# Kernel tuning notes

Hardware: AMD Instinct MI355X
Metric: run time of the kernel (lower is better)

Reference implementation:

```python
import jax, jax.numpy as jnp
import numpy as np

DIM = 128; DSTATE = 64; DHEAD = 64; EXPAND = 2
DINNER = EXPAND * DIM; NH = DINNER // DHEAD
CONVK = 4; CHUNK = 128
BATCH = 1; DD = 32; HH = 32; WW = 32
CONVCH = DINNER + 2 * DSTATE
DPROJ = 2 * DINNER + 2 * DSTATE + NH


def rmsnorm(v, w, eps=1e-6):
    return v * jax.lax.rsqrt(jnp.mean(v * v, axis=-1, keepdims=True) + eps) * w


def ssd(xh, dt, A, Bm, Cm):
    # chunked SSD selective scan. xh [b,l,h,p], dt [b,l,h], A [h], Bm/Cm [b,l,n]
    b, l, h, p = xh.shape
    n = Bm.shape[-1]
    c, k = l // CHUNK, CHUNK
    dA = (dt * A).reshape(b, c, k, h)
    xdt = (xh * dt[..., None]).reshape(b, c, k, h, p)
    Bm = Bm.reshape(b, c, k, n)
    Cm = Cm.reshape(b, c, k, n)
    cum = jnp.cumsum(dA, axis=2)                  # [b,c,k,h] inclusive
    cum_h = cum.transpose(0, 1, 3, 2)             # [b,c,h,k]
    tri = jnp.tril(jnp.ones((k, k), bool))
    Lmat = jnp.exp(jnp.where(tri, cum_h[..., :, None] - cum_h[..., None, :], -jnp.inf))
    CB = jnp.einsum('bctn,bcsn->bcts', Cm, Bm)
    Y_intra = jnp.einsum('bcts,bchts,bcshp->bcthp', CB, Lmat, xdt)
    decay_end = jnp.exp(cum[:, :, -1:, :] - cum)  # [b,c,k,h]
    S = jnp.einsum('bcsn,bcsh,bcshp->bchpn', Bm, decay_end, xdt)
    cdec = jnp.exp(cum[:, :, -1])                 # [b,c,h]

    def step(hprev, inp):
        s_c, dec = inp
        return dec[:, :, None, None] * hprev + s_c, hprev

    init = jnp.zeros((b, h, p, n), xh.dtype)
    _, hprevs = jax.lax.scan(step, init, (S.transpose(1, 0, 2, 3, 4), cdec.transpose(1, 0, 2)))
    hprevs = hprevs.transpose(1, 0, 2, 3, 4)      # [b,c,h,p,n] state at each chunk start
    Y_inter = jnp.einsum('bctn,bcth,bchpn->bcthp', Cm, jnp.exp(cum), hprevs)
    return (Y_intra + Y_inter).reshape(b, l, h, p)


def mamba2(x, Win, convw, convb, dtb, Alog, Dp, normw, Wout):
    b, l, _ = x.shape
    zxbcdt = x @ Win
    z = zxbcdt[..., :DINNER]
    xBC = zxbcdt[..., DINNER:DINNER + CONVCH]
    dt = zxbcdt[..., DINNER + CONVCH:]
    xc = xBC.transpose(0, 2, 1)
    xc = jax.lax.conv_general_dilated(xc, convw, (1,), [(CONVK - 1, 0)],
                                      dimension_numbers=('NCH', 'OIH', 'NCH'),
                                      feature_group_count=CONVCH)
    xBC = jax.nn.silu(xc + convb[None, :, None]).transpose(0, 2, 1)
    xh = xBC[..., :DINNER].reshape(b, l, NH, DHEAD)
    Bm = xBC[..., DINNER:DINNER + DSTATE]
    Cm = xBC[..., DINNER + DSTATE:]
    dt = jax.nn.softplus(dt + dtb)
    A = -jnp.exp(Alog)
    y = ssd(xh, dt, A, Bm, Cm) + Dp[None, None, :, None] * xh
    y = y.reshape(b, l, DINNER)
    y = rmsnorm(y * jax.nn.silu(z), normw)
    return y @ Wout


def ss3d(xn, gate_w, gate_b, ps, pn, pz):
    B, D, H, W, C = xn.shape
    x_s = xn.reshape(B, -1, C)
    x_n = jnp.transpose(xn, (0, 2, 1, 3, 4)).reshape(B, -1, C)
    x_z = jnp.transpose(xn, (0, 3, 1, 2, 4)).reshape(B, -1, C)
    o_sf = mamba2(x_s, *ps).reshape(B, D, H, W, C)
    o_sb = jnp.flip(mamba2(jnp.flip(x_s, 1), *ps), 1).reshape(B, D, H, W, C)
    o_nf = mamba2(x_n, *pn).reshape(B, H, D, W, C).transpose(0, 2, 1, 3, 4)
    o_nb = jnp.flip(mamba2(jnp.flip(x_n, 1), *pn), 1).reshape(B, H, D, W, C).transpose(0, 2, 1, 3, 4)
    o_zf = mamba2(x_z, *pz).reshape(B, W, D, H, C).transpose(0, 2, 3, 1, 4)
    o_zb = jnp.flip(mamba2(jnp.flip(x_z, 1), *pz), 1).reshape(B, W, D, H, C).transpose(0, 2, 3, 1, 4)
    stack = jnp.stack([o_sf, o_sb, o_nf, o_nb, o_zf, o_zb], axis=1)  # [B,6,D,H,W,C]
    gates = jax.nn.softmax(xn @ gate_w + gate_b, axis=-1)            # [B,D,H,W,6]
    gates = jnp.transpose(gates[..., None], (0, 4, 1, 2, 3, 5))      # [B,6,D,H,W,1]
    return (stack * gates).sum(axis=1)


def block(x, norm_w, gate_w, gate_b, ps, pn, pz, loc_dw_w, loc_dw_b, loc_pw_w, loc_pw_b,
          ca_w1, ca_b1, ca_w2, ca_b2, alpha):
    xp = jnp.transpose(x, (0, 2, 3, 4, 1))
    xn = rmsnorm(xp, norm_w)
    g = jnp.transpose(ss3d(xn, gate_w, gate_b, ps, pn, pz), (0, 4, 1, 2, 3))
    xcf = jnp.transpose(xn, (0, 4, 1, 2, 3))
    lc = jax.lax.conv_general_dilated(xcf, loc_dw_w, (1, 1, 1), [(1, 1)] * 3,
                                      dimension_numbers=('NCDHW', 'OIDHW', 'NCDHW'),
                                      feature_group_count=DIM) + loc_dw_b[None, :, None, None, None]
    lc = jax.nn.silu(jnp.einsum('bcdhw,oc->bodhw', lc, loc_pw_w) + loc_pw_b[None, :, None, None, None])
    fused = alpha * g + (1.0 - alpha) * lc
    yc = jnp.mean(fused, axis=(2, 3, 4), keepdims=True)
    yc = jnp.einsum('bcdhw,oc->bodhw', yc, ca_w1) + ca_b1[None, :, None, None, None]
    yc = jnp.where(yc >= 0, yc, 0.1 * yc)  # LeakyReLU(0.1)
    yc = jnp.einsum('bcdhw,oc->bodhw', yc, ca_w2) + ca_b2[None, :, None, None, None]
    return x + fused * jax.nn.sigmoid(yc)


def setup_inputs() -> dict:
    keys = iter(jax.random.split(jax.random.key(0), 64))

    def rn(shape, s=1.0):
        return jax.random.normal(next(keys), shape, jnp.float32) * s

    inp = {"x": rn((BATCH, DIM, DD, HH, WW))}
    inp["norm_w"] = jnp.ones((DIM,)) + rn((DIM,), 0.02)
    inp["gate_w"] = rn((DIM, 6), 0.02)
    inp["gate_b"] = jnp.zeros((6,))
    for m in ("s", "n", "zm"):
        inp[m + "_Win"] = rn((DIM, DPROJ), 0.02)
        inp[m + "_convw"] = rn((CONVCH, 1, CONVK), 0.2)
        inp[m + "_convb"] = jnp.zeros((CONVCH,))
        inp[m + "_dtb"] = rn((NH,), 0.3)
        inp[m + "_Alog"] = jnp.log(jnp.arange(1, NH + 1, dtype=jnp.float32))
        inp[m + "_D"] = jnp.ones((NH,))
        inp[m + "_normw"] = jnp.ones((DINNER,))
        inp[m + "_Wout"] = rn((DINNER, DIM), 0.02)
    inp["loc_dw_w"] = rn((DIM, 1, 3, 3, 3), 0.1)
    inp["loc_dw_b"] = jnp.zeros((DIM,))
    inp["loc_pw_w"] = rn((DIM, DIM), 0.05)
    inp["loc_pw_b"] = jnp.zeros((DIM,))
    inp["ca_w1"] = rn((DIM // 16, DIM), 0.05)
    inp["ca_b1"] = jnp.zeros((DIM // 16,))
    inp["ca_w2"] = rn((DIM, DIM // 16), 0.05)
    inp["ca_b2"] = jnp.zeros((DIM,))
    inp["alpha"] = jnp.array(0.5, jnp.float32)
    return inp


def reference(x, norm_w, gate_w, gate_b,
              s_Win, s_convw, s_convb, s_dtb, s_Alog, s_D, s_normw, s_Wout,
              n_Win, n_convw, n_convb, n_dtb, n_Alog, n_D, n_normw, n_Wout,
              zm_Win, zm_convw, zm_convb, zm_dtb, zm_Alog, zm_D, zm_normw, zm_Wout,
              loc_dw_w, loc_dw_b, loc_pw_w, loc_pw_b, ca_w1, ca_b1, ca_w2, ca_b2, alpha):
    ps = (s_Win, s_convw, s_convb, s_dtb, s_Alog, s_D, s_normw, s_Wout)
    pn = (n_Win, n_convw, n_convb, n_dtb, n_Alog, n_D, n_normw, n_Wout)
    pz = (zm_Win, zm_convw, zm_convb, zm_dtb, zm_Alog, zm_D, zm_normw, zm_Wout)
    return block(x, norm_w, gate_w, gate_b, ps, pn, pz,
                 loc_dw_w, loc_dw_b, loc_pw_w, loc_pw_b, ca_w1, ca_b1, ca_w2, ca_b2, alpha)
```

## Files before the change

### kernel.cpp

```cpp
#include <hip/hip_runtime.h>


typedef unsigned short u16;
typedef unsigned int   u32;
typedef __attribute__((ext_vector_type(8))) short short8;
typedef __attribute__((ext_vector_type(8))) _Float16 half8;
typedef __attribute__((ext_vector_type(4))) float f32x4;

#define LSEQ 32768
#define CDIM 128
#define NPROJ 644
#define ZXS 672
#define CCH 384
#define DIN 256
#define NHD 4
#define CKL 128
#define NCHK 256

__device__ __forceinline__ float b2f(u16 u){ u32 x=((u32)u)<<16; float f; __builtin_memcpy(&f,&x,4); return f; }
__device__ __forceinline__ u16 f2b(float f){ u32 x; __builtin_memcpy(&x,&f,4); x += 0x7fffu + ((x>>16)&1u); return (u16)(x>>16); }
__device__ __forceinline__ u16 f2h(float v){ _Float16 h=(_Float16)v; u16 b; __builtin_memcpy(&b,&h,2); return b; }
__device__ __forceinline__ float h2f(u16 b){ _Float16 h; __builtin_memcpy(&h,&b,2); return (float)h; }
__device__ __forceinline__ void up4(uint2 v, float* o){
  union { uint2 u; _Float16 h[4]; } c; c.u = v;
  o[0]=(float)c.h[0]; o[1]=(float)c.h[1]; o[2]=(float)c.h[2]; o[3]=(float)c.h[3];
}
__device__ __forceinline__ uint2 pk4(const float* o){
  union { uint2 u; _Float16 h[4]; } c;
  c.h[0]=(_Float16)o[0]; c.h[1]=(_Float16)o[1]; c.h[2]=(_Float16)o[2]; c.h[3]=(_Float16)o[3];
  return c.u;
}
__device__ __forceinline__ float sigmoidf_(float v){ return 1.f/(1.f+__expf(-v)); }
__device__ __forceinline__ float siluf_(float v){ return v*sigmoidf_(v); }
__device__ __forceinline__ float softplusf_(float v){ return (v>20.f)? v : log1pf(__expf(v)); }

__device__ __forceinline__ int seq2sp(int t, int run){
  int te = (run&1) ? (LSEQ-1-t) : t;
  int a = te>>10, b=(te>>5)&31, c=te&31;
  int d,h,w;
  switch(run>>1){
    case 0: d=a; h=b; w=c; break;
    case 1: h=a; d=b; w=c; break;
    default: w=a; d=b; h=c; break;
  }
  return (d<<10)|(h<<5)|w;
}

__global__ void k_xn(const float* __restrict__ x, const float* __restrict__ nw,
                     const float* __restrict__ gw, const float* __restrict__ gb,
                     float* __restrict__ XN, float* __restrict__ G){
  int s = blockIdx.x*256 + threadIdx.x;
  float ss = 0.f;
  #pragma unroll 8
  for (int c=0;c<CDIM;c++){ float v=x[c*LSEQ+s]; ss += v*v; }
  float sc = rsqrtf(ss*(1.f/CDIM)+1e-6f);
  float a[6];
  #pragma unroll
  for (int j=0;j<6;j++) a[j]=gb[j];
  #pragma unroll 8
  for (int c=0;c<CDIM;c++){
    float v = x[c*LSEQ+s]*sc*nw[c];
    XN[c*LSEQ+s] = v;
    #pragma unroll
    for (int j=0;j<6;j++) a[j] += v*gw[c*6+j];
  }
  float m=a[0];
  #pragma unroll
  for (int j=1;j<6;j++) m = fmaxf(m,a[j]);
  float e[6], ssum=0.f;
  #pragma unroll
  for (int j=0;j<6;j++){ e[j]=__expf(a[j]-m); ssum+=e[j]; }
  float inv = 1.f/ssum;
  #pragma unroll
  for (int j=0;j<6;j++) G[j*LSEQ+s] = e[j]*inv;
}

__global__ __launch_bounds__(256) void k_permprep(const float* __restrict__ XN, u16* __restrict__ XNT, int dir,
                                                  const float* __restrict__ Win, const float* __restrict__ Wout,
                                                  u16* __restrict__ WinT, u16* __restrict__ WoT){
  __shared__ u16 TS[128*34];
  int bid = blockIdx.x;
  int tid = threadIdx.x;
  if (bid < 1024){
    int a = bid>>5, b = bid&31;
    int spa = (dir==1)? b : a;
    int spb = (dir==1)? a : b;
    int spbase = spa*1024 + spb*32;
    for (int idx=tid; idx<4096; idx+=256){
      int c = idx>>5, i = idx&31;
      TS[c*34+i] = f2b(XN[c*LSEQ + spbase + i]);
    }
    __syncthreads();
    for (int idx=tid; idx<4096; idx+=256){
      int i = idx>>7, c = idx&127;
      int t = (dir==2) ? (i*1024 + a*32 + b) : (a*1024 + b*32 + i);
      XNT[t*128 + c] = TS[c*34+i];
    }
  } else if (bid < 1408){
    int idx = (bid-1024)*256 + tid;
    int j = idx>>7, k = idx&127;
    float v = (j<NPROJ)? Win[k*NPROJ + j] : 0.f;
    WinT[idx] = f2b(v);
  } else {
    int idx = (bid-1408)*256 + tid;
    int c = idx>>8, k = idx&255;
    WoT[idx] = f2h(Wout[k*CDIM + c]);
  }
}

__global__ __launch_bounds__(256) void k_gin_mfma(const u16* __restrict__ XNT, const u16* __restrict__ WinT,
                                                  u16* __restrict__ ZX, int flip){
  __shared__ u16 Asb[128*136];
  __shared__ u16 Bsb[128*136];
  int g = blockIdx.x;
  int w = (g&7)*192 + (g>>3);
  int by = w/6, bx = w - by*6;
  int j0 = bx*128, t0 = by*128;
  int tid = threadIdx.x;
  for (int ch = tid; ch < 2048; ch += 256){
    int row = ch>>4, c8 = ch&15;
    int tg = flip ? (LSEQ-1-(t0+row)) : (t0+row);
    uint4 av = *(const uint4*)(XNT + tg*128 + c8*8);
    *(uint4*)(&Asb[row*136 + c8*8]) = av;
    uint4 bv = *(const uint4*)(WinT + (j0+row)*128 + c8*8);
    *(uint4*)(&Bsb[row*136 + c8*8]) = bv;
  }
  __syncthreads();
  int lane = tid&63, wid = tid>>6;
  int wm = (wid>>1)*64, wn = (wid&1)*64;
  int lm = lane&15, lq = lane>>4;
  f32x4 acc[4][4] = {};
  for (int kt=0; kt<4; kt++){
    short8 af[4], bf[4];
    #pragma unroll
    for (int mt=0;mt<4;mt++) af[mt] = *(const short8*)(&Asb[(wm+mt*16+lm)*136 + kt*32 + lq*8]);
    #pragma unroll
    for (int nt=0;nt<4;nt++) bf[nt] = *(const short8*)(&Bsb[(wn+nt*16+lm)*136 + kt*32 + lq*8]);
    #pragma unroll
    for (int mt=0;mt<4;mt++)
      #pragma unroll
      for (int nt=0;nt<4;nt++)
        acc[mt][nt] = __builtin_amdgcn_mfma_f32_16x16x32_bf16(af[mt], bf[nt], acc[mt][nt], 0,0,0);
  }
  __syncthreads();
  #pragma unroll
  for (int mt=0;mt<4;mt++)
    #pragma unroll
    for (int nt=0;nt<4;nt++)
      #pragma unroll
      for (int r=0;r<4;r++)
        Asb[(wm+mt*16+lq*4+r)*136 + wn+nt*16+lm] = f2h(acc[mt][nt][r]);
  __syncthreads();
  if (bx < 5){
    for (int idx=tid; idx<2048; idx+=256){
      int row = idx>>4, q = idx&15;
      *(uint4*)(ZX + (t0+row)*ZXS + j0 + q*8) = *(const uint4*)(&Asb[row*136 + q*8]);
    }
  } else {
    for (int idx=tid; idx<128; idx+=256){
      *(uint2*)(ZX + (t0+idx)*ZXS + j0) = *(const uint2*)(&Asb[idx*136]);
    }
  }
}

__global__ __launch_bounds__(384) void k_convdt(const u16* __restrict__ ZX, const float* __restrict__ cw,
                                                const float* __restrict__ cb, u16* __restrict__ XB,
                                                const float* __restrict__ dtb, const float* __restrict__ Alog,
                                                float* __restrict__ DT, float* __restrict__ CUM,
                                                float* __restrict__ CDEC, float* __restrict__ DE){
  __shared__ u16 smc[35*384];
  int bid = blockIdx.x;
  int tid = threadIdx.x;
  if (bid < 1024){
    int t0 = bid*32;
    for (int idx=tid; idx<13440; idx+=384){
      int j = idx/384, chh = idx - j*384;
      int t = t0-3+j;
      smc[idx] = (t>=0)? ZX[t*ZXS + 256 + chh] : (u16)0;
    }
    __syncthreads();
    int ch = tid;
    float w0=cw[ch*4], w1=cw[ch*4+1], w2=cw[ch*4+2], w3=cw[ch*4+3], bb=cb[ch];
    for (int i=0;i<32;i++){
      float acc = w0*h2f(smc[i*384+ch]) + w1*h2f(smc[(i+1)*384+ch])
                + w2*h2f(smc[(i+2)*384+ch]) + w3*h2f(smc[(i+3)*384+ch]) + bb;
      XB[(t0+i)*CCH + ch] = f2h(siluf_(acc));
    }
  } else if (tid < 256){
    int g = (bid-1024)*4 + (tid>>6);
    int lane = tid&63;
    int c = g>>2, h = g&3;
    float A = -__expf(Alog[h]);
    float bias = dtb[h];
    int t0 = c*CKL + lane*2;
    float x0 = h2f(ZX[t0*ZXS + 640 + h]);
    float x1 = h2f(ZX[(t0+1)*ZXS + 640 + h]);
    float d0 = softplusf_(x0+bias), d1 = softplusf_(x1+bias);
    DT[t0*4+h] = d0; DT[(t0+1)*4+h] = d1;
    float e0 = d0*A, e1 = d1*A;
    float s = e0+e1;
    #pragma unroll
    for (int off=1; off<64; off<<=1){
      float v = __shfl_up(s, off, 64);
      if (lane>=off) s += v;
    }
    float c0 = s - e1, c1 = s;
    CUM[t0*4+h] = c0;
    CUM[(t0+1)*4+h] = c1;
    float tot = __shfl(s, 63, 64);
    DE[t0*4+h]     = __expf(tot - c0);
    DE[(t0+1)*4+h] = __expf(tot - c1);
    if (lane==0) CDEC[c*4+h] = __expf(tot);
  }
}

__global__ __launch_bounds__(256,4) void k_chunk(const u16* __restrict__ XB, const float* __restrict__ DT,
                                                 const float* __restrict__ CUM, const float* __restrict__ DE,
                                                 const float* __restrict__ Dp,
                                                 u16* __restrict__ YA, u16* __restrict__ ST){
  __shared__ u16 sh[19968];
  u16* R0   = sh;
  u16* Mtri = sh;
  u16* Xsh  = sh + 11264;
  u16* scr  = sh;

  int bid = blockIdx.x; int c = bid&255, h = bid>>8;
  int tid = threadIdx.x, lane = tid&63, wid = tid>>6;
  int lm = lane&15, lq = lane>>4;
  const u16* XBc = XB + c*CKL*CCH;
  const float* DTc = DT + c*CKL*4 + h;
  const float* DEc = DE + c*CKL*4 + h;

  for (int idx=tid; idx<4096; idx+=256){
    int t2 = idx>>6, n = idx&63, t = t2*2;
    const u16* r0 = XBc + t*CCH;
    float dt0 = DTc[t*4], dt1 = DTc[(t+1)*4];
    u32 xp = (u32)f2h(h2f(r0[(h<<6)+n])*dt0) | ((u32)f2h(h2f(r0[CCH+(h<<6)+n])*dt1)<<16);
    *(u32*)&Xsh[n*136 + t] = xp;
    float de0 = DEc[t*4], de1 = DEc[(t+1)*4];
    u32 bp = (u32)f2h(h2f(r0[256+n])*de0) | ((u32)f2h(h2f(r0[CCH+256+n])*de1)<<16);
    *(u32*)&R0[n*136 + t] = bp;
  }
  if (tid<128) ((float*)(Xsh + (tid>>1)*136 + 128))[tid&1] = CUM[(c*CKL+tid)*4 + h];
  __syncthreads();
  #define CUMS(t) (((const float*)(Xsh + ((t)>>1)*136 + 128))[(t)&1])

  f32x4 sa[4] = {};
  #pragma unroll
  for (int kt=0; kt<4; kt++){
    half8 aa = *(const half8*)&Xsh[(wid*16+lm)*136 + kt*32 + lq*8];
    #pragma unroll
    for (int nt=0;nt<4;nt++){
      half8 bq = *(const half8*)&R0[(nt*16+lm)*136 + kt*32 + lq*8];
      sa[nt] = __builtin_amdgcn_mfma_f32_16x16x32_f16(aa, bq, sa[nt], 0,0,0);
    }
  }
  #pragma unroll
  for (int nt=0;nt<4;nt++){
    int n = nt*16 + lm;
    #pragma unroll
    for (int r=0;r<4;r++){
      int p = wid*16 + lq*4 + r;
      ST[((c*4+h)*64 + p)*64 + n] = f2h(sa[nt][r]);
    }
  }

  int sp0 = wid, sp1 = 7 - wid;
  f32x4 cbA[4] = {};
  f32x4 cbB[8] = {};
  const u16* lanebase = XBc + lm*CCH + lq*8;
  #pragma unroll
  for (int kt=0; kt<2; kt++){
    half8 afA = *(const half8*)(lanebase + sp0*16*CCH + 320 + kt*32);
    half8 afB = *(const half8*)(lanebase + sp1*16*CCH + 320 + kt*32);
    #pragma unroll
    for (int st=0; st<8; st++){
      if (st <= sp1){
        half8 bq = *(const half8*)(lanebase + st*16*CCH + 256 + kt*32);
        if (st <= sp0)
          cbA[st&3] = __builtin_amdgcn_mfma_f32_16x16x32_f16(afA, bq, cbA[st&3], 0,0,0);
        cbB[st] = __builtin_amdgcn_mfma_f32_16x16x32_f16(afB, bq, cbB[st], 0,0,0);
      }
    }
  }
  __syncthreads();

  float dval = Dp[h];
  u16 outv[2][4][4];
  #pragma unroll
  for (int i=0;i<2;i++){
    int sp_ = i ? sp1 : sp0;
    int q = sp_ >> 1;
    int Wst = 32*q + 40;
    int mb  = 16*(32*q*q + 48*q + (sp_&1)*(32*q+40));
    u16* Mrow = Mtri + mb;
    float ct[4];
    #pragma unroll
    for (int r=0;r<4;r++) ct[r] = CUMS(sp_*16 + lq*4 + r);

    #pragma unroll
    for (int st=0; st<8; st++){
      if (st <= sp_){
        int s = st*16 + lm;
        float cs = CUMS(s);
        f32x4 cb;
        if (i==0) cb = cbA[st&3]; else cb = cbB[st];
        if (st == sp_){
          #pragma unroll
          for (int r=0;r<4;r++){
            int t = sp_*16 + lq*4 + r;
            float m = (s <= t) ? cb[r]*__expf(ct[r]-cs) : 0.f;
            Mrow[(lq*4+r)*Wst + s] = f2h(m);
          }
          if (!(sp_&1)){
            #pragma unroll
            for (int r=0;r<4;r++) Mrow[(lq*4+r)*Wst + s + 16] = 0;
          }
        } else {
          #pragma unroll
          for (int r=0;r<4;r++)
            Mrow[(lq*4+r)*Wst + s] = f2h(cb[r]*__expf(ct[r]-cs));
        }
      }
    }

    f32x4 ya[4] = {};
    int nkt = q + 1;
    #pragma unroll
    for (int kt=0; kt<4; kt++){
      if (kt < nkt){
        half8 af = *(const half8*)&Mrow[lm*Wst + kt*32 + lq*8];
        #pragma unroll
        for (int nt=0;nt<4;nt++){
          half8 bq = *(const half8*)&Xsh[(nt*16+lm)*136 + kt*32 + lq*8];
          ya[nt] = __builtin_amdgcn_mfma_f32_16x16x32_f16(af, bq, ya[nt], 0,0,0);
        }
      }
    }

    #pragma unroll
    for (int nt=0;nt<4;nt++){
      int p = nt*16 + lm;
      #pragma unroll
      for (int r=0;r<4;r++){
        int t = sp_*16 + lq*4 + r;
        float xhv = h2f(XBc[t*CCH + (h<<6) + p]);
        outv[i][nt][r] = f2h(ya[nt][r] + dval*xhv);
      }
    }
  }
  __syncthreads();

  #pragma unroll
  for (int i=0;i<2;i++){
    int sp_ = i ? sp1 : sp0;
    #pragma unroll
    for (int nt=0;nt<4;nt++)
      #pragma unroll
      for (int r=0;r<4;r++)
        scr[(sp_*16+lq*4+r)*68 + nt*16+lm] = outv[i][nt][r];
  }
  __syncthreads();
  for (int idx=tid; idx<2048; idx+=256){
    int row = idx>>4, q = idx&15;
    *(uint2*)(YA + ((c*CKL+row)<<8) + (h<<6) + q*4) = *(const uint2*)(&scr[row*68 + q*4]);
  }
  #undef CUMS
}

__global__ __launch_bounds__(256) void k_scan(const u16* __restrict__ ST, u16* __restrict__ HP,
                                              const float* __restrict__ CDEC){
  __shared__ float L[4][64][64];
  __shared__ float E[4][64];
  int tid = threadIdx.x;
  int j = tid>>6, s = tid&63;
  int b = blockIdx.x;
  int g = b*64 + s;
  int h = g>>12;
  int a = j*64;
  float hloc = 0.f;
  #pragma unroll 16
  for (int i=0;i<64;i++){
    int c = a+i;
    L[j][i][s] = hloc;
    hloc = CDEC[(c<<2)+h]*hloc + h2f(ST[g + (c<<14)]);
  }
  E[j][s] = hloc;
  __syncthreads();
  float carry = 0.f;
  for (int k=0;k<j;k++){
    float P = 1.f;
    #pragma unroll 16
    for (int i=0;i<64;i++) P *= CDEC[((k*64+i)<<2)+h];
    carry = E[k][s] + P*carry;
  }
  float m = 1.f;
  #pragma unroll 16
  for (int i=0;i<64;i++){
    int c = a+i;
    HP[g + (c<<14)] = f2h(L[j][i][s] + m*carry);
    m *= CDEC[(c<<2)+h];
  }
}

__global__ __launch_bounds__(256) void k_inter(const u16* __restrict__ XB, const float* __restrict__ CUM,
                                               const u16* __restrict__ HP, u16* __restrict__ YB){
  __shared__ u16 Cs[128*72];
  __shared__ u16 Hs[4*64*72];
  __shared__ float ex_s[4*128];
  int c = blockIdx.x;
  int tid = threadIdx.x, lane = tid&63, wid = tid>>6;
  int lm = lane&15, lq = lane>>4;
  for (int idx=tid; idx<1024; idx+=256){
    int t = idx>>3, b8 = idx&7;
    *(uint4*)&Cs[t*72 + b8*8] = *(const uint4*)(XB + (c*CKL+t)*CCH + 320 + b8*8);
  }
  for (int idx=tid; idx<2048; idx+=256){
    int h = idx>>9, p = (idx>>3)&63, b8 = idx&7;
    *(uint4*)&Hs[(h*64+p)*72 + b8*8] = *(const uint4*)(HP + ((c*4+h)*64+p)*64 + b8*8);
  }
  for (int idx=tid; idx<512; idx+=256){
    int h = idx>>7, t = idx&127;
    ex_s[h*128+t] = __expf(CUM[(c*CKL+t)*4+h]);
  }
  __syncthreads();
  int h = wid;
  const u16* Hh = &Hs[h*64*72];
  f32x4 acc[8][4] = {};
  for (int kt=0; kt<2; kt++){
    half8 af[8], bfv[4];
    #pragma unroll
    for (int mt=0;mt<8;mt++) af[mt] = *(const half8*)&Cs[(mt*16+lm)*72 + kt*32 + lq*8];
    #pragma unroll
    for (int nt=0;nt<4;nt++) bfv[nt] = *(const half8*)&Hh[(nt*16+lm)*72 + kt*32 + lq*8];
    #pragma unroll
    for (int mt=0;mt<8;mt++)
      #pragma unroll
      for (int nt=0;nt<4;nt++)
        acc[mt][nt] = __builtin_amdgcn_mfma_f32_16x16x32_f16(af[mt], bfv[nt], acc[mt][nt], 0,0,0);
  }
  #pragma unroll
  for (int mt=0;mt<8;mt++){
    #pragma unroll
    for (int r=0;r<4;r++){
      int t = mt*16 + lq*4 + r;
      float e = ex_s[h*128+t];
      u16* dst = &YB[((c*CKL+t)<<8) + (h<<6)];
      #pragma unroll
      for (int nt=0;nt<4;nt++){
        int p = nt*16 + lm;
        dst[p] = f2h(e*acc[mt][nt][r]);
      }
    }
  }
}

__global__ __launch_bounds__(256) void k_gout_mfma(const u16* __restrict__ YA, const u16* __restrict__ YB,
                                                   const u16* __restrict__ ZX, const float* __restrict__ nw,
                                                   const u16* __restrict__ WoT,
                                                   const float* __restrict__ G, float* __restrict__ GACC, int run){
  __shared__ u16 Ys[128*136];
  __shared__ u16 Ws[128*136];
  __shared__ float SSs[128];
  int t0 = blockIdx.x*128;
  int tid = threadIdx.x, lane = tid&63, wid = tid>>6;
  int lm = lane&15, lq = lane>>4;
  f32x4 acc[2][8] = {};
  for (int kb=0; kb<2; kb++){
    __syncthreads();
    for (int ch=tid; ch<2048; ch+=256){
      int row = ch>>4, c8 = ch&15;
      int t = t0+row;
      int cb = kb*128 + c8*8;
      uint2 av0 = *(const uint2*)(YA + t*DIN + cb);
      uint2 av1 = *(const uint2*)(YA + t*DIN + cb + 4);
      uint2 bv0 = *(const uint2*)(YB + t*DIN + cb);
      uint2 bv1 = *(const uint2*)(YB + t*DIN + cb + 4);
      uint2 zv0 = *(const uint2*)(ZX + t*ZXS + cb);
      uint2 zv1 = *(const uint2*)(ZX + t*ZXS + cb + 4);
      float af[8], bf[8], zf[8];
      up4(av0, af); up4(av1, af+4);
      up4(bv0, bf); up4(bv1, bf+4);
      up4(zv0, zf); up4(zv1, zf+4);
      float ssp = 0.f;
      union { uint4 u; u16 h[8]; } pk;
      #pragma unroll
      for (int j=0;j<8;j++){
        float u = (af[j]+bf[j])*siluf_(zf[j]);
        ssp += u*u;
        pk.h[j] = f2h(u*nw[cb+j]);
      }
      *(uint4*)&Ys[row*136 + c8*8] = pk.u;
      *(uint4*)&Ws[row*136 + c8*8] = *(const uint4*)(WoT + row*DIN + kb*128 + c8*8);
      #pragma unroll
      for (int off=1; off<16; off<<=1) ssp += __shfl_xor(ssp, off, 64);
      if ((lane&15)==0){ if (kb==0) SSs[row] = ssp; else SSs[row] += ssp; }
    }
    __syncthreads();
    for (int kt=0; kt<4; kt++){
      half8 af[2], bfv[8];
      #pragma unroll
      for (int mt=0;mt<2;mt++) af[mt] = *(const half8*)&Ys[(wid*32+mt*16+lm)*136 + kt*32 + lq*8];
      #pragma unroll
      for (int nt=0;nt<8;nt++) bfv[nt] = *(const half8*)&Ws[(nt*16+lm)*136 + kt*32 + lq*8];
      #pragma unroll
      for (int mt=0;mt<2;mt++)
        #pragma unroll
        for (int nt=0;nt<8;nt++)
          acc[mt][nt] = __builtin_amdgcn_mfma_f32_16x16x32_f16(af[mt], bfv[nt], acc[mt][nt], 0,0,0);
    }
  }
  #pragma unroll
  for (int mt=0;mt<2;mt++){
    #pragma unroll
    for (int r=0;r<4;r++){
      int tl = wid*32 + mt*16 + lq*4 + r;
      int t = t0 + tl;
      int sp = seq2sp(t, run);
      float sc = rsqrtf(SSs[tl]*(1.f/DIN)+1e-6f);
      float g = G[run*LSEQ + sp] * sc;
      float* dst = &GACC[sp*CDIM];
      if (run==0){
        #pragma unroll
        for (int nt=0;nt<8;nt++) dst[nt*16+lm] = g*acc[mt][nt][r];
      } else {
        #pragma unroll
        for (int nt=0;nt<8;nt++) dst[nt*16+lm] += g*acc[mt][nt][r];
      }
    }
  }
}

__global__ __launch_bounds__(256) void k_dwconv(const float* __restrict__ XN, const float* __restrict__ w,
                                                const float* __restrict__ b, float* __restrict__ LC1){
  __shared__ float sm[3*34*40];
  int cc = blockIdx.x>>5, d = blockIdx.x&31;
  int tid = threadIdx.x;
  for (int i=tid; i<4080; i+=256) sm[i] = 0.f;
  __syncthreads();
  #pragma unroll
  for (int p=0;p<3;p++){
    int dz = d-1+p;
    if ((unsigned)dz<=31u){
      for (int idx=tid; idx<1024; idx+=256){
        int hh = idx>>5, ww = idx&31;
        sm[p*1360 + (hh+1)*40 + (ww+4)] = XN[cc*LSEQ + (dz<<10) + idx];
      }
    }
  }
  __syncthreads();
  float wreg[27];
  #pragma unroll
  for (int i=0;i<27;i++) wreg[i] = w[cc*27+i];
  float bias = b[cc];
  int h = tid>>3, w0 = (tid&7)*4;
  float4 acc = {bias,bias,bias,bias};
  #pragma unroll
  for (int p=0;p<3;p++){
    #pragma unroll
    for (int dy=0;dy<3;dy++){
      const float* row = &sm[p*1360 + (h+dy)*40 + 4];
      float left  = row[w0-1];
      float4 mid  = *(const float4*)&row[w0];
      float right = row[w0+4];
      float wa=wreg[p*9+dy*3+0], wb=wreg[p*9+dy*3+1], wc=wreg[p*9+dy*3+2];
      acc.x += wa*left  + wb*mid.x + wc*mid.y;
      acc.y += wa*mid.x + wb*mid.y + wc*mid.z;
      acc.z += wa*mid.y + wb*mid.z + wc*mid.w;
      acc.w += wa*mid.z + wb*mid.w + wc*right;
    }
  }
  *(float4*)&LC1[cc*LSEQ + (d<<10) + h*32 + w0] = acc;
}

__global__ __launch_bounds__(256) void k_pw(const float* __restrict__ LC1, const float* __restrict__ pw,
                                            const float* __restrict__ pwb, float* __restrict__ LC2){
  __shared__ u16 Ws[128*136];
  __shared__ u16 Bs[128*136];
  int s0 = blockIdx.x*128;
  int tid = threadIdx.x, lane = tid&63, wid = tid>>6;
  int lm = lane&15, lq = lane>>4;
  for (int idx=tid; idx<16384; idx+=256){
    int o = idx>>7, cc = idx&127;
    Ws[o*136+cc] = f2h(pw[idx]);
  }
  for (int idx=tid; idx<16384; idx+=256){
    int cc = idx>>7, n = idx&127;
    Bs[n*136+cc] = f2h(LC1[cc*LSEQ + s0 + n]);
  }
  __syncthreads();
  f32x4 acc[2][8] = {};
  for (int kt=0; kt<4; kt++){
    half8 af[2], bfv[8];
    #pragma unroll
    for (int mt=0;mt<2;mt++) af[mt] = *(const half8*)&Ws[(wid*32+mt*16+lm)*136 + kt*32 + lq*8];
    #pragma unroll
    for (int nt=0;nt<8;nt++) bfv[nt] = *(const half8*)&Bs[(nt*16+lm)*136 + kt*32 + lq*8];
    #pragma unroll
    for (int mt=0;mt<2;mt++)
      #pragma unroll
      for (int nt=0;nt<8;nt++)
        acc[mt][nt] = __builtin_amdgcn_mfma_f32_16x16x32_f16(af[mt], bfv[nt], acc[mt][nt], 0,0,0);
  }
  #pragma unroll
  for (int mt=0;mt<2;mt++){
    #pragma unroll
    for (int r=0;r<4;r++){
      int o = wid*32 + mt*16 + lq*4 + r;
      float bb = pwb[o];
      float* dst = &LC2[o*LSEQ + s0];
      #pragma unroll
      for (int nt=0;nt<8;nt++){
        int n = nt*16 + lm;
        dst[n] = siluf_(acc[mt][nt][r] + bb);
      }
    }
  }
}

__global__ void k_fuse(const float* __restrict__ GACC, const float* __restrict__ LC2,
                       const float* __restrict__ alpha, float* __restrict__ FUSED,
                       float* __restrict__ MEANP){
  __shared__ float tile[64*65];
  int bs = blockIdx.x>>1, bc = blockIdx.x&1;
  int s0 = bs*64, c0 = bc*64;
  int tid = threadIdx.x;
  float a = alpha[0];
  for (int idx=tid; idx<4096; idx+=256){
    int i = idx>>6, j = idx&63;
    tile[i*65+j] = GACC[(s0+i)*CDIM + c0+j];
  }
  __syncthreads();
  for (int idx=tid; idx<4096; idx+=256){
    int j = idx>>6, i = idx&63;
    float g = tile[i*65+j];
    float l = LC2[(c0+j)*LSEQ + s0+i];
    float f = a*g + (1.f-a)*l;
    FUSED[(c0+j)*LSEQ + s0+i] = f;
    float wsum = f;
    #pragma unroll
    for (int off=32; off; off>>=1) wsum += __shfl_xor(wsum, off, 64);
    if ((tid&63)==0) MEANP[(c0+j)*512 + bs] = wsum;
  }
}

__global__ void k_ca(const float* __restrict__ MEANP, const float* __restrict__ w1, const float* __restrict__ b1,
                     const float* __restrict__ w2, const float* __restrict__ b2, float* __restrict__ SIG){
  __shared__ float MEANsh[128];
  __shared__ float y1[8];
  int tid = threadIdx.x;
  {
    float acc = 0.f;
    const float* p = MEANP + tid*512;
    #pragma unroll 16
    for (int b=0;b<512;b++) acc += p[b];
    MEANsh[tid] = acc*(1.f/LSEQ);
  }
  __syncthreads();
  if (tid<8){
    float acc = b1[tid];
    for (int c=0;c<128;c++) acc += w1[tid*128+c]*MEANsh[c];
    y1[tid] = (acc>=0.f)? acc : 0.1f*acc;
  }
  __syncthreads();
  float acc = b2[tid];
  #pragma unroll
  for (int o=0;o<8;o++) acc += w2[tid*8+o]*y1[o];
  SIG[tid] = sigmoidf_(acc);
}

__global__ void k_final(const float* __restrict__ x, const float* __restrict__ F, const float* __restrict__ SIG,
                        float* __restrict__ out){
  int idx = blockIdx.x*256 + threadIdx.x;
  int cc = idx>>15;
  out[idx] = x[idx] + F[idx]*SIG[cc];
}

extern "C" void kernel_launch(void* const* d_in, const int* in_sizes, int n_in,
                              void* d_out, int out_size, void* d_ws, size_t ws_size,
                              hipStream_t stream){
  (void)in_sizes; (void)n_in; (void)out_size; (void)ws_size;
  const float* x       = (const float*)d_in[0];
  const float* norm_w  = (const float*)d_in[1];
  const float* gate_w  = (const float*)d_in[2];
  const float* gate_b  = (const float*)d_in[3];
  const float* loc_dw_w= (const float*)d_in[28];
  const float* loc_dw_b= (const float*)d_in[29];
  const float* loc_pw_w= (const float*)d_in[30];
  const float* loc_pw_b= (const float*)d_in[31];
  const float* ca_w1   = (const float*)d_in[32];
  const float* ca_b1   = (const float*)d_in[33];
  const float* ca_w2   = (const float*)d_in[34];
  const float* ca_b2   = (const float*)d_in[35];
  const float* alpha   = (const float*)d_in[36];

  float* W     = (float*)d_ws;
  float* XN    = W;
  float* GATES = XN    + 4194304;
  float* GACC  = GATES + 196608;
  u16*   ZX    = (u16*)(GACC + 4194304);
  u16*   XB    = (u16*)(GACC + 4194304 + 11010048);
  float* DT    = GACC + 4194304 + 11010048 + 6291456;
  float* CUM   = DT    + 131072;
  float* CDEC  = CUM   + 131072;
  float* DE    = CDEC  + 1024;
  float* STreg = DE    + 131072;
  float* Y     = STreg + 4194304;
  float* LC1   = Y     + 8388608;
  float* LC2   = LC1   + 4194304;
  float* MEANP = LC2   + 4194304;
  float* SIG   = MEANP + 65536;
  u16*   XNT   = (u16*)(SIG + 128);
  u16*   WinT  = XNT + 4194304;
  u16*   WoT   = WinT + 98304;
  u16*   ST16  = (u16*)STreg;
  u16*   YA    = (u16*)Y;
  u16*   YB    = YA + 8388608;
  u16*   HP16  = (u16*)LC1;

  k_xn<<<128,256,0,stream>>>(x, norm_w, gate_w, gate_b, XN, GATES);

  for (int r=0;r<6;r++){
    int m = r>>1;
    const float* Win   = (const float*)d_in[4 + m*8 + 0];
    const float* convw = (const float*)d_in[4 + m*8 + 1];
    const float* convb = (const float*)d_in[4 + m*8 + 2];
    const float* dtb   = (const float*)d_in[4 + m*8 + 3];
    const float* Alog  = (const float*)d_in[4 + m*8 + 4];
    const float* Dp    = (const float*)d_in[4 + m*8 + 5];
    const float* nw2   = (const float*)d_in[4 + m*8 + 6];
    const float* Wout  = (const float*)d_in[4 + m*8 + 7];
    if ((r&1)==0){
      k_permprep<<<1536,256,0,stream>>>(XN, XNT, m, Win, Wout, WinT, WoT);
    }
    k_gin_mfma<<<1536,256,0,stream>>>(XNT, WinT, ZX, r&1);
    k_convdt  <<<1280,384,0,stream>>>(ZX, convw, convb, XB, dtb, Alog, DT, CUM, CDEC, DE);
    k_chunk   <<<1024,256,0,stream>>>(XB, DT, CUM, DE, Dp, YA, ST16);
    k_scan    <<<256,256,0,stream>>>(ST16, HP16, CDEC);
    k_inter   <<<256,256,0,stream>>>(XB, CUM, HP16, YB);
    k_gout_mfma<<<256,256,0,stream>>>(YA, YB, ZX, nw2, WoT, GATES, GACC, r);
  }

  k_dwconv<<<4096,256,0,stream>>>(XN, loc_dw_w, loc_dw_b, LC1);
  k_pw    <<<256,256,0,stream>>>(LC1, loc_pw_w, loc_pw_b, LC2);
  k_fuse  <<<1024,256,0,stream>>>(GACC, LC2, alpha, LC1, MEANP);
  k_ca    <<<1,128,0,stream>>>(MEANP, ca_w1, ca_b1, ca_w2, ca_b2, SIG);
  k_final <<<16384,256,0,stream>>>(x, LC1, SIG, (float*)d_out);
}
```

Before: 910.5 us.

## Fuse inter-chunk output kernel with gated norm and output projection

Merges k_inter and k_gout_mfma into one kernel, so the inter-chunk Y contribution stays in shared memory instead of being written to and re-read from a global YB buffer. Shared memory is aliased between phases, and the second half of heads is staged after the first kb pass. WoT fragments are now read directly from global memory rather than staged in LDS. This saves one launch and a large fp16 round trip per run. The costs are extra syncs, higher register pressure from holding both accumulators, and uncached global B-operand loads.

```diff
diff --git a/kernel.cpp b/kernel.cpp
--- a/kernel.cpp
+++ b/kernel.cpp
@@ -403,17 +403,26 @@
   }
 }
 
-__global__ __launch_bounds__(256) void k_inter(const u16* __restrict__ XB, const float* __restrict__ CUM,
-                                               const u16* __restrict__ HP, u16* __restrict__ YB){
-  __shared__ u16 Cs[128*72];
-  __shared__ u16 Hs[4*64*72];
-  __shared__ float ex_s[4*128];
+__global__ __launch_bounds__(256,2) void k_intergout(const u16* __restrict__ XB, const float* __restrict__ CUM,
+                                                     const u16* __restrict__ HP,
+                                                     const u16* __restrict__ YA, const u16* __restrict__ ZX,
+                                                     const float* __restrict__ nw, const u16* __restrict__ WoT,
+                                                     const float* __restrict__ G, float* __restrict__ GACC, int run){
+  __shared__ u16 sh[34304];
+  __shared__ float ex_s[512];
+  __shared__ float SSs[128];
+  u16* Cs  = sh;
+  u16* Hs  = sh + 9216;
+  u16* Ybs = sh;
+  u16* Ys  = sh + 16896;
   int c = blockIdx.x;
   int tid = threadIdx.x, lane = tid&63, wid = tid>>6;
   int lm = lane&15, lq = lane>>4;
+  int t0 = c*CKL;
+
   for (int idx=tid; idx<1024; idx+=256){
     int t = idx>>3, b8 = idx&7;
-    *(uint4*)&Cs[t*72 + b8*8] = *(const uint4*)(XB + (c*CKL+t)*CCH + 320 + b8*8);
+    *(uint4*)&Cs[t*72 + b8*8] = *(const uint4*)(XB + (t0+t)*CCH + 320 + b8*8);
   }
   for (int idx=tid; idx<2048; idx+=256){
     int h = idx>>9, p = (idx>>3)&63, b8 = idx&7;
@@ -421,111 +430,119 @@
   }
   for (int idx=tid; idx<512; idx+=256){
     int h = idx>>7, t = idx&127;
-    ex_s[h*128+t] = __expf(CUM[(c*CKL+t)*4+h]);
-  }
-  __syncthreads();
-  int h = wid;
-  const u16* Hh = &Hs[h*64*72];
-  f32x4 acc[8][4] = {};
-  for (int kt=0; kt<2; kt++){
-    half8 af[8], bfv[4];
-    #pragma unroll
-    for (int mt=0;mt<8;mt++) af[mt] = *(const half8*)&Cs[(mt*16+lm)*72 + kt*32 + lq*8];
-    #pragma unroll
-    for (int nt=0;nt<4;nt++) bfv[nt] = *(const half8*)&Hh[(nt*16+lm)*72 + kt*32 + lq*8];
-    #pragma unroll
-    for (int mt=0;mt<8;mt++)
-      #pragma unroll
-      for (int nt=0;nt<4;nt++)
-        acc[mt][nt] = __builtin_amdgcn_mfma_f32_16x16x32_f16(af[mt], bfv[nt], acc[mt][nt], 0,0,0);
-  }
-  #pragma unroll
-  for (int mt=0;mt<8;mt++){
-    #pragma unroll
-    for (int r=0;r<4;r++){
-      int t = mt*16 + lq*4 + r;
-      float e = ex_s[h*128+t];
-      u16* dst = &YB[((c*CKL+t)<<8) + (h<<6)];
-      #pragma unroll
-      for (int nt=0;nt<4;nt++){
-        int p = nt*16 + lm;
-        dst[p] = f2h(e*acc[mt][nt][r]);
-      }
-    }
-  }
-}
-
-__global__ __launch_bounds__(256) void k_gout_mfma(const u16* __restrict__ YA, const u16* __restrict__ YB,
-                                                   const u16* __restrict__ ZX, const float* __restrict__ nw,
-                                                   const u16* __restrict__ WoT,
-                                                   const float* __restrict__ G, float* __restrict__ GACC, int run){
-  __shared__ u16 Ys[128*136];
-  __shared__ u16 Ws[128*136];
-  __shared__ float SSs[128];
-  int t0 = blockIdx.x*128;
-  int tid = threadIdx.x, lane = tid&63, wid = tid>>6;
-  int lm = lane&15, lq = lane>>4;
-  f32x4 acc[2][8] = {};
-  for (int kb=0; kb<2; kb++){
+    ex_s[h*128+t] = __expf(CUM[(t0+t)*4+h]);
+  }
+  __syncthreads();
+
+  {
+    const u16* Hh = &Hs[wid*64*72];
+    f32x4 iacc[8][4] = {};
+    for (int kt=0; kt<2; kt++){
+      half8 af[8], bfv[4];
+      #pragma unroll
+      for (int mt=0;mt<8;mt++) af[mt] = *(const half8*)&Cs[(mt*16+lm)*72 + kt*32 + lq*8];
+      #pragma unroll
+      for (int nt=0;nt<4;nt++) bfv[nt] = *(const half8*)&Hh[(nt*16+lm)*72 + kt*32 + lq*8];
+      #pragma unroll
+      for (int mt=0;mt<8;mt++)
+        #pragma unroll
+        for (int nt=0;nt<4;nt++)
+          iacc[mt][nt] = __builtin_amdgcn_mfma_f32_16x16x32_f16(af[mt], bfv[nt], iacc[mt][nt], 0,0,0);
+    }
     __syncthreads();
-    for (int ch=tid; ch<2048; ch+=256){
-      int row = ch>>4, c8 = ch&15;
-      int t = t0+row;
-      int cb = kb*128 + c8*8;
-      uint2 av0 = *(const uint2*)(YA + t*DIN + cb);
-      uint2 av1 = *(const uint2*)(YA + t*DIN + cb + 4);
-      uint2 bv0 = *(const uint2*)(YB + t*DIN + cb);
-      uint2 bv1 = *(const uint2*)(YB + t*DIN + cb + 4);
-      uint2 zv0 = *(const uint2*)(ZX + t*ZXS + cb);
-      uint2 zv1 = *(const uint2*)(ZX + t*ZXS + cb + 4);
-      float af[8], bf[8], zf[8];
-      up4(av0, af); up4(av1, af+4);
-      up4(bv0, bf); up4(bv1, bf+4);
-      up4(zv0, zf); up4(zv1, zf+4);
-      float ssp = 0.f;
-      union { uint4 u; u16 h[8]; } pk;
-      #pragma unroll
-      for (int j=0;j<8;j++){
-        float u = (af[j]+bf[j])*siluf_(zf[j]);
-        ssp += u*u;
-        pk.h[j] = f2h(u*nw[cb+j]);
-      }
-      *(uint4*)&Ys[row*136 + c8*8] = pk.u;
-      *(uint4*)&Ws[row*136 + c8*8] = *(const uint4*)(WoT + row*DIN + kb*128 + c8*8);
-      #pragma unroll
-      for (int off=1; off<16; off<<=1) ssp += __shfl_xor(ssp, off, 64);
-      if ((lane&15)==0){ if (kb==0) SSs[row] = ssp; else SSs[row] += ssp; }
+
+    if (wid < 2){
+      #pragma unroll
+      for (int mt=0;mt<8;mt++){
+        #pragma unroll
+        for (int r=0;r<4;r++){
+          int t = mt*16 + lq*4 + r;
+          float e = ex_s[wid*128+t];
+          #pragma unroll
+          for (int nt=0;nt<4;nt++)
+            Ybs[t*132 + wid*64 + nt*16+lm] = f2h(e*iacc[mt][nt][r]);
+        }
+      }
     }
     __syncthreads();
-    for (int kt=0; kt<4; kt++){
-      half8 af[2], bfv[8];
-      #pragma unroll
-      for (int mt=0;mt<2;mt++) af[mt] = *(const half8*)&Ys[(wid*32+mt*16+lm)*136 + kt*32 + lq*8];
-      #pragma unroll
-      for (int nt=0;nt<8;nt++) bfv[nt] = *(const half8*)&Ws[(nt*16+lm)*136 + kt*32 + lq*8];
-      #pragma unroll
-      for (int mt=0;mt<2;mt++)
+
+    f32x4 acc[2][8] = {};
+    for (int kb=0; kb<2; kb++){
+      for (int ch=tid; ch<2048; ch+=256){
+        int row = ch>>4, c8 = ch&15;
+        int t = t0+row;
+        int cb = kb*128 + c8*8;
+        uint2 av0 = *(const uint2*)(YA + t*DIN + cb);
+        uint2 av1 = *(const uint2*)(YA + t*DIN + cb + 4);
+        uint2 bv0 = *(const uint2*)&Ybs[row*132 + c8*8];
+        uint2 bv1 = *(const uint2*)&Ybs[row*132 + c8*8 + 4];
+        uint2 zv0 = *(const uint2*)(ZX + t*ZXS + cb);
+        uint2 zv1 = *(const uint2*)(ZX + t*ZXS + cb + 4);
+        float af[8], bf[8], zf[8];
+        up4(av0, af); up4(av1, af+4);
+        up4(bv0, bf); up4(bv1, bf+4);
+        up4(zv0, zf); up4(zv1, zf+4);
+        float ssp = 0.f;
+        union { uint4 u; u16 h[8]; } pk;
         #pragma unroll
-        for (int nt=0;nt<8;nt++)
-          acc[mt][nt] = __builtin_amdgcn_mfma_f32_16x16x32_f16(af[mt], bfv[nt], acc[mt][nt], 0,0,0);
-    }
-  }
-  #pragma unroll
-  for (int mt=0;mt<2;mt++){
-    #pragma unroll
-    for (int r=0;r<4;r++){
-      int tl = wid*32 + mt*16 + lq*4 + r;
-      int t = t0 + tl;
-      int sp = seq2sp(t, run);
-      float sc = rsqrtf(SSs[tl]*(1.f/DIN)+1e-6f);
-      float g = G[run*LSEQ + sp] * sc;
-      float* dst = &GACC[sp*CDIM];
-      if (run==0){
+        for (int j=0;j<8;j++){
+          float u = (af[j]+bf[j])*siluf_(zf[j]);
+          ssp += u*u;
+          pk.h[j] = f2h(u*nw[cb+j]);
+        }
+        *(uint4*)&Ys[row*136 + c8*8] = pk.u;
         #pragma unroll
-        for (int nt=0;nt<8;nt++) dst[nt*16+lm] = g*acc[mt][nt][r];
-      } else {
+        for (int off=1; off<16; off<<=1) ssp += __shfl_xor(ssp, off, 64);
+        if ((lane&15)==0){ if (kb==0) SSs[row] = ssp; else SSs[row] += ssp; }
+      }
+      __syncthreads();
+      for (int kt=0; kt<4; kt++){
+        half8 af[2], bfv[8];
         #pragma unroll
-        for (int nt=0;nt<8;nt++) dst[nt*16+lm] += g*acc[mt][nt][r];
+        for (int mt=0;mt<2;mt++) af[mt] = *(const half8*)&Ys[(wid*32+mt*16+lm)*136 + kt*32 + lq*8];
+        #pragma unroll
+        for (int nt=0;nt<8;nt++) bfv[nt] = *(const half8*)(WoT + (nt*16+lm)*DIN + kb*128 + kt*32 + lq*8);
+        #pragma unroll
+        for (int mt=0;mt<2;mt++)
+          #pragma unroll
+          for (int nt=0;nt<8;nt++)
+            acc[mt][nt] = __builtin_amdgcn_mfma_f32_16x16x32_f16(af[mt], bfv[nt], acc[mt][nt], 0,0,0);
+      }
+      if (kb==0){
+        if (wid >= 2){
+          #pragma unroll
+          for (int mt=0;mt<8;mt++){
+            #pragma unroll
+            for (int r=0;r<4;r++){
+              int t = mt*16 + lq*4 + r;
+              float e = ex_s[wid*128+t];
+              #pragma unroll
+              for (int nt=0;nt<4;nt++)
+                Ybs[t*132 + (wid-2)*64 + nt*16+lm] = f2h(e*iacc[mt][nt][r]);
+            }
+          }
+        }
+        __syncthreads();
+      }
+    }
+
+    #pragma unroll
+    for (int mt=0;mt<2;mt++){
+      #pragma unroll
+      for (int r=0;r<4;r++){
+        int tl = wid*32 + mt*16 + lq*4 + r;
+        int t = t0 + tl;
+        int sp = seq2sp(t, run);
+        float sc = rsqrtf(SSs[tl]*(1.f/DIN)+1e-6f);
+        float g = G[run*LSEQ + sp] * sc;
+        float* dst = &GACC[sp*CDIM];
+        if (run==0){
+          #pragma unroll
+          for (int nt=0;nt<8;nt++) dst[nt*16+lm] = g*acc[mt][nt][r];
+        } else {
+          #pragma unroll
+          for (int nt=0;nt<8;nt++) dst[nt*16+lm] += g*acc[mt][nt][r];
+        }
       }
     }
   }
@@ -715,7 +732,6 @@
   u16*   WoT   = WinT + 98304;
   u16*   ST16  = (u16*)STreg;
   u16*   YA    = (u16*)Y;
-  u16*   YB    = YA + 8388608;
   u16*   HP16  = (u16*)LC1;
 
   k_xn<<<128,256,0,stream>>>(x, norm_w, gate_w, gate_b, XN, GATES);
@@ -737,8 +753,7 @@
     k_convdt  <<<1280,384,0,stream>>>(ZX, convw, convb, XB, dtb, Alog, DT, CUM, CDEC, DE);
     k_chunk   <<<1024,256,0,stream>>>(XB, DT, CUM, DE, Dp, YA, ST16);
     k_scan    <<<256,256,0,stream>>>(ST16, HP16, CDEC);
-    k_inter   <<<256,256,0,stream>>>(XB, CUM, HP16, YB);
-    k_gout_mfma<<<256,256,0,stream>>>(YA, YB, ZX, nw2, WoT, GATES, GACC, r);
+    k_intergout<<<256,256,0,stream>>>(XB, CUM, HP16, YA, ZX, nw2, WoT, GATES, GACC, r);
   }
 
   k_dwconv<<<4096,256,0,stream>>>(XN, loc_dw_w, loc_dw_b, LC1);
```

Result: slower. 952.5 us (+4.6%).
